# Optimization experiments

Measured on AMD Instinct MI355X. Metric: run time of the kernel, lower is better.

The kernel has to match this reference:

```python
import jax, jax.numpy as jnp
import numpy as np

EPS = 1e-8

def elu_feature_map(x):
    return jax.nn.elu(x) + 1.0

def setup_inputs() -> dict:
    key = jax.random.key(0)
    ks = jax.random.split(key, 5)
    B, S, D = 2, 4096, 1024
    scale = 1.0 / np.sqrt(D).astype(np.float32)
    x = jax.random.normal(ks[0], (B, S, D), dtype=jnp.float32)
    Wq = jax.random.normal(ks[1], (D, D), dtype=jnp.float32) * scale
    Wk = jax.random.normal(ks[2], (D, D), dtype=jnp.float32) * scale
    Wv = jax.random.normal(ks[3], (D, D), dtype=jnp.float32) * scale
    Wo = jax.random.normal(ks[4], (D, D), dtype=jnp.float32) * scale
    return {"x": x, "Wq": Wq, "Wk": Wk, "Wv": Wv, "Wo": Wo}

def reference(x, Wq, Wk, Wv, Wo):
    B, S, D = x.shape
    H = 16
    Dh = D // H
    # projections (nn.Linear with no bias: x @ W.T)
    def proj(W):
        return (x @ W.T).reshape(B, S, H, Dh)
    q = elu_feature_map(proj(Wq))  # [B,S,H,Dh]
    k = elu_feature_map(proj(Wk))
    v = proj(Wv)
    # scan over sequence: carry running kv_sum [B,H,Dh,Dh] and k_sum [B,H,Dh]
    q_t = jnp.moveaxis(q, 1, 0)  # [S,B,H,Dh]
    k_t = jnp.moveaxis(k, 1, 0)
    v_t = jnp.moveaxis(v, 1, 0)

    def step(carry, qkv):
        kv_sum, k_sum = carry
        q_i, k_i, v_i = qkv  # each [B,H,Dh]
        kv_sum = kv_sum + jnp.einsum('bhd,bhe->bhde', k_i, v_i)
        k_sum = k_sum + k_i
        num = jnp.einsum('bhd,bhde->bhe', q_i, kv_sum)
        den = jnp.sum(q_i * k_sum, axis=-1, keepdims=True)
        out_i = num / (den + EPS)
        return (kv_sum, k_sum), out_i

    kv0 = jnp.zeros((B, H, Dh, Dh), dtype=x.dtype)
    ks0 = jnp.zeros((B, H, Dh), dtype=x.dtype)
    _, out = jax.lax.scan(step, (kv0, ks0), (q_t, k_t, v_t))  # out: [S,B,H,Dh]
    out = jnp.moveaxis(out, 0, 1).reshape(B, S, D)
    return out @ Wo.T
```

## Files before the change

kernel.cpp:

```cpp
#include <hip/hip_runtime.h>
#include <math.h>


#define EPSF 1e-8f

typedef unsigned short u16;
typedef unsigned int   u32;
typedef __attribute__((ext_vector_type(8))) short short8v;
typedef __attribute__((ext_vector_type(4))) float f32x4;

__device__ __forceinline__ float elu1(float x){ return x > 0.f ? x + 1.f : __expf(x); }
__device__ __forceinline__ u16 f2bf(float f){
    union{float f; u32 i;} c; c.f = f;
    u32 i = c.i + 0x7FFFu + ((c.i >> 16) & 1u);
    return (u16)(i >> 16);
}
__device__ __forceinline__ float bf2f(u16 v){ union{u32 i; float f;} c; c.i = (u32)v << 16; return c.f; }
__device__ __forceinline__ float bflo(u32 v){ union{u32 i; float f;} c; c.i = v << 16; return c.f; }
__device__ __forceinline__ float bfhi(u32 v){ union{u32 i; float f;} c; c.i = v & 0xffff0000u; return c.f; }
__device__ __forceinline__ void f4a(float4 v, float* a){ a[0]=v.x; a[1]=v.y; a[2]=v.z; a[3]=v.w; }

__device__ __forceinline__ void gload16(const void* g, void* l){
    __builtin_amdgcn_global_load_lds((const __attribute__((address_space(1))) u32*)g,
                                     (__attribute__((address_space(3))) u32*)l, 16, 0, 0);
}

__global__ __launch_bounds__(256) void k_cast5(
    const float* __restrict__ x,  const float* __restrict__ wq,
    const float* __restrict__ wk, const float* __restrict__ wv,
    const float* __restrict__ wo,
    u16* __restrict__ xb, u16* __restrict__ wcat, u16* __restrict__ wob)
{
    size_t i8 = ((size_t)blockIdx.x * 256 + threadIdx.x) * 8;
    const float* s; u16* d; size_t off;
    if      (i8 <  8388608) { s = x;  d = xb;            off = i8; }
    else if (i8 <  9437184) { s = wq; d = wcat;          off = i8 - 8388608; }
    else if (i8 < 10485760) { s = wk; d = wcat + 1048576; off = i8 - 9437184; }
    else if (i8 < 11534336) { s = wv; d = wcat + 2097152; off = i8 - 10485760; }
    else                    { s = wo; d = wob;           off = i8 - 11534336; }
    float4 a = *(const float4*)&s[off];
    float4 b = *(const float4*)&s[off + 4];
    uint4 p;
    p.x = (u32)f2bf(a.x) | ((u32)f2bf(a.y) << 16);
    p.y = (u32)f2bf(a.z) | ((u32)f2bf(a.w) << 16);
    p.z = (u32)f2bf(b.x) | ((u32)f2bf(b.y) << 16);
    p.w = (u32)f2bf(b.z) | ((u32)f2bf(b.w) << 16);
    *(uint4*)&d[off] = p;
}

template<int MODE, int NBY>
__global__ __launch_bounds__(256, 3) void k_gemm9(
    const u16* __restrict__ Ag, const u16* __restrict__ Wg, void* __restrict__ Cv)
{
    __shared__ __align__(16) char dsm[49152];
    const int bid = blockIdx.x;
    const int nid = (bid & 7) * ((64 * NBY) >> 3) + (bid >> 3);
    const int bx  = nid / NBY;
    const int by  = nid % NBY;
    const int m0  = bx * 128;
    const int n0  = by * 128;

    const int tid = threadIdx.x;
    const int l   = tid & 63;
    const int wid = tid >> 6;
    const int wm  = wid >> 1;
    const int wn  = wid & 1;
    const int li  = l & 15;
    const int kgi = l >> 4;

    const int ra0 = wm*64 + li;
    const int offA0 = ((ra0 >> 1) << 7) + (((((ra0 & 1) << 2) | kgi) ^ ((ra0 >> 1) & 7)) << 4);
    const int rb0 = wn*64 + li;
    const int offB0 = ((rb0 >> 1) << 7) + (((((rb0 & 1) << 2) | kgi) ^ ((rb0 >> 1) & 7)) << 4);

    const int sx   = (l & 7) ^ (l >> 3);
    const int rowb = 2*(wid*8 + (l >> 3)) + (sx >> 2);
    const int skg  = (sx & 3) * 8;
    const u16* srcA = Ag + (size_t)(m0 + rowb) * 1024 + skg;
    const u16* srcB = Wg + (size_t)(n0 + rowb) * 1024 + skg;

    f32x4 acc[4][4];
    #pragma unroll
    for (int m = 0; m < 4; ++m)
        #pragma unroll
        for (int n = 0; n < 4; ++n) acc[m][n] = (f32x4){0.f, 0.f, 0.f, 0.f};

    #define ST9(BUF, T) { \
        char* ab = dsm + (BUF)*16384; \
        char* bb = ab + 8192; \
        _Pragma("unroll") for (int j = 0; j < 2; ++j) \
            gload16(srcA + (size_t)j*65536 + (T)*32, ab + j*4096 + wid*1024); \
        _Pragma("unroll") for (int j = 0; j < 2; ++j) \
            gload16(srcB + (size_t)j*65536 + (T)*32, bb + j*4096 + wid*1024); }

    #define CP9(BUF) { \
        const char* Ab = dsm + (BUF)*16384; \
        const char* Bb = Ab + 8192; \
        short8v bfr[4]; \
        _Pragma("unroll") for (int n = 0; n < 4; ++n) bfr[n] = *(const short8v*)(Bb + offB0 + n*1024); \
        __builtin_amdgcn_s_setprio(1); \
        _Pragma("unroll") for (int m = 0; m < 4; ++m) { \
            short8v afr = *(const short8v*)(Ab + offA0 + m*1024); \
            _Pragma("unroll") for (int n = 0; n < 4; ++n) \
                acc[m][n] = __builtin_amdgcn_mfma_f32_16x16x32_bf16(afr, bfr[n], acc[m][n], 0, 0, 0); \
        } \
        __builtin_amdgcn_s_setprio(0); }

    #define STEP9(CUR, STB, TS) { \
        ST9(STB, TS); \
        CP9(CUR); \
        asm volatile("s_waitcnt vmcnt(4)"); \
        __builtin_amdgcn_s_barrier(); }

    ST9(0, 0); ST9(1, 1);
    asm volatile("s_waitcnt vmcnt(4)");
    __builtin_amdgcn_s_barrier();

    #pragma unroll 1
    for (int g = 0; g < 10; ++g) {
        const int t = g * 3;
        STEP9(0, 2, t + 2);
        STEP9(1, 0, t + 3);
        STEP9(2, 1, t + 4);
    }
    CP9(0);
    asm volatile("s_waitcnt vmcnt(0)");
    __builtin_amdgcn_s_barrier();
    CP9(1);
    #undef STEP9
    #undef CP9
    #undef ST9

    const int r0 = m0 + wm*64 + kgi*4;
    if (MODE == 1) {
        const int matrix = by >> 3;
        const bool do_elu = matrix < 2;
        u16* outp = (u16*)Cv + (size_t)matrix * 8388608;
        const int c0 = (by & 7)*128 + wn*64 + li;
        #pragma unroll
        for (int m = 0; m < 4; ++m)
            #pragma unroll
            for (int n = 0; n < 4; ++n)
                #pragma unroll
                for (int r = 0; r < 4; ++r) {
                    float v = acc[m][n][r];
                    if (do_elu) v = elu1(v);
                    outp[(size_t)(r0 + m*16 + r) * 1024 + c0 + n*16] = f2bf(v);
                }
    } else {
        float* outp = (float*)Cv;
        const int c0 = by*128 + wn*64 + li;
        #pragma unroll
        for (int m = 0; m < 4; ++m)
            #pragma unroll
            for (int n = 0; n < 4; ++n)
                #pragma unroll
                for (int r = 0; r < 4; ++r)
                    outp[(size_t)(r0 + m*16 + r) * 1024 + c0 + n*16] = acc[m][n][r];
    }
}

__global__ __launch_bounds__(256) void k_chunksums(
    const u16* __restrict__ Kg, const u16* __restrict__ Vg,
    u16* __restrict__ CKVb, float* __restrict__ CKS)
{
    const int tid = threadIdx.x;
    const int tx = tid & 15, ty = tid >> 4;
    const int c  = blockIdx.x & 63;
    const int bh = blockIdx.x >> 6;
    const int b = bh >> 4, h = bh & 15;
    const int row0 = b * 4096 + c * 64;
    const int col  = h * 64;

    __shared__ float Ks[64][68];
    __shared__ float Vs[64][68];

    #pragma unroll
    for (int r = 0; r < 2; ++r) {
        int idx = tid + r * 256;
        int i = idx >> 3, cg = (idx & 7) << 3;
        uint4 ku = *(const uint4*)&Kg[(size_t)(row0 + i) * 1024 + col + cg];
        uint4 vu = *(const uint4*)&Vg[(size_t)(row0 + i) * 1024 + col + cg];
        Ks[i][cg+0]=bflo(ku.x); Ks[i][cg+1]=bfhi(ku.x);
        Ks[i][cg+2]=bflo(ku.y); Ks[i][cg+3]=bfhi(ku.y);
        Ks[i][cg+4]=bflo(ku.z); Ks[i][cg+5]=bfhi(ku.z);
        Ks[i][cg+6]=bflo(ku.w); Ks[i][cg+7]=bfhi(ku.w);
        Vs[i][cg+0]=bflo(vu.x); Vs[i][cg+1]=bfhi(vu.x);
        Vs[i][cg+2]=bflo(vu.y); Vs[i][cg+3]=bfhi(vu.y);
        Vs[i][cg+4]=bflo(vu.z); Vs[i][cg+5]=bfhi(vu.z);
        Vs[i][cg+6]=bflo(vu.w); Vs[i][cg+7]=bfhi(vu.w);
    }
    __syncthreads();

    float acc[4][4] = {};
    #pragma unroll 8
    for (int i = 0; i < 64; ++i) {
        float kv[4], vv[4];
        f4a(*(const float4*)&Ks[i][ty*4], kv);
        f4a(*(const float4*)&Vs[i][tx*4], vv);
        #pragma unroll
        for (int a = 0; a < 4; ++a)
            #pragma unroll
            for (int e = 0; e < 4; ++e)
                acc[a][e] = fmaf(kv[a], vv[e], acc[a][e]);
    }
    u16* ckv = &CKVb[(size_t)blockIdx.x * 4096];
    #pragma unroll
    for (int e = 0; e < 4; ++e) {
        u32 p0 = (u32)f2bf(acc[0][e]) | ((u32)f2bf(acc[1][e]) << 16);
        u32 p1 = (u32)f2bf(acc[2][e]) | ((u32)f2bf(acc[3][e]) << 16);
        *(uint2*)&ckv[(tx*4 + e) * 64 + ty*4] = make_uint2(p0, p1);
    }

    if (tid < 64) {
        float s = 0.f;
        #pragma unroll 8
        for (int i = 0; i < 64; ++i) s += Ks[i][tid];
        CKS[(size_t)blockIdx.x * 64 + tid] = s;
    }
}

__global__ __launch_bounds__(256) void k_prefix(u16* __restrict__ CKV, float* __restrict__ CKS)
{
    if (blockIdx.x < 512) {
        const int bh = blockIdx.x >> 4;
        const int p  = ((blockIdx.x & 15) << 8) + threadIdx.x;
        const size_t base = (size_t)bh * 64 * 4096 + p;
        float acc = 0.f;
        #pragma unroll
        for (int c = 0; c < 64; ++c) {
            float t = bf2f(CKV[base + (size_t)c * 4096]);
            CKV[base + (size_t)c * 4096] = f2bf(acc);
            acc += t;
        }
    } else {
        const int idx = (blockIdx.x - 512) * 256 + threadIdx.x;
        const int bh = idx >> 6, d = idx & 63;
        const size_t base = (size_t)bh * 64 * 64 + d;
        float v[64];
        #pragma unroll
        for (int c = 0; c < 64; ++c) v[c] = CKS[base + (size_t)c * 64];
        float acc = 0.f;
        #pragma unroll
        for (int c = 0; c < 64; ++c) { float t = v[c]; CKS[base + (size_t)c * 64] = acc; acc += t; }
    }
}

#define LSTR 72
__global__ __launch_bounds__(256) void k_attn2(
    const u16* __restrict__ Qg, const u16* __restrict__ Kg, const u16* __restrict__ Vg,
    const u16* __restrict__ Stg, const float* __restrict__ KSg, u16* __restrict__ AO)
{
    const int tid = threadIdx.x;
    const int l = tid & 63;
    const int w = tid >> 6;
    const int c  = blockIdx.x & 63;
    const int bh = blockIdx.x >> 6;
    const int row0 = (bh >> 4) * 4096 + c * 64;
    const int col  = (bh & 15) * 64;

    __shared__ __align__(16) u16 Qs [64 * LSTR];
    __shared__ __align__(16) u16 Ks [64 * LSTR];
    __shared__ __align__(16) u16 Vt [64 * LSTR];
    __shared__ __align__(16) u16 Sts[64 * LSTR];
    __shared__ __align__(16) u16 Pl [64 * LSTR];
    __shared__ float ksumF[64];
    __shared__ float invdenL[64];

    #pragma unroll
    for (int r = 0; r < 2; ++r) {
        int idx = tid + r * 256;
        int i = idx >> 3, cg = (idx & 7) << 3;
        *(uint4*)&Qs [i*LSTR + cg] = *(const uint4*)&Qg [(size_t)(row0 + i) * 1024 + col + cg];
        *(uint4*)&Ks [i*LSTR + cg] = *(const uint4*)&Kg [(size_t)(row0 + i) * 1024 + col + cg];
        *(uint4*)&Sts[i*LSTR + cg] = *(const uint4*)&Stg[(size_t)blockIdx.x * 4096 + i * 64 + cg];
        uint4 vu = *(const uint4*)&Vg[(size_t)(row0 + i) * 1024 + col + cg];
        Vt[(cg+0)*LSTR + i] = (u16)(vu.x & 0xffff);
        Vt[(cg+1)*LSTR + i] = (u16)(vu.x >> 16);
        Vt[(cg+2)*LSTR + i] = (u16)(vu.y & 0xffff);
        Vt[(cg+3)*LSTR + i] = (u16)(vu.y >> 16);
        Vt[(cg+4)*LSTR + i] = (u16)(vu.z & 0xffff);
        Vt[(cg+5)*LSTR + i] = (u16)(vu.z >> 16);
        Vt[(cg+6)*LSTR + i] = (u16)(vu.w & 0xffff);
        Vt[(cg+7)*LSTR + i] = (u16)(vu.w >> 16);
    }
    if (tid < 64) ksumF[tid] = KSg[(size_t)blockIdx.x * 64 + tid];
    __syncthreads();

    const int li = l & 15;
    const int lg = l >> 4;
    const int i_row = w * 16 + li;

    short8v bq[2];
    #pragma unroll
    for (int kc = 0; kc < 2; ++kc)
        bq[kc] = *(const short8v*)&Qs[i_row * LSTR + lg*8 + kc*32];

    float den = EPSF;
    #pragma unroll
    for (int mj = 0; mj < 4; ++mj) {
        f32x4 sacc = (f32x4){0.f, 0.f, 0.f, 0.f};
        #pragma unroll
        for (int kc = 0; kc < 2; ++kc) {
            short8v ak = *(const short8v*)&Ks[(mj*16 + li) * LSTR + lg*8 + kc*32];
            sacc = __builtin_amdgcn_mfma_f32_16x16x32_bf16(ak, bq[kc], sacc, 0, 0, 0);
        }
        const int jbase = mj*16 + lg*4;
        float pv[4];
        #pragma unroll
        for (int r = 0; r < 4; ++r) {
            float v = sacc[r];
            v = (jbase + r <= i_row) ? v : 0.f;
            den += v;
            pv[r] = v;
        }
        u32 lo = (u32)f2bf(pv[0]) | ((u32)f2bf(pv[1]) << 16);
        u32 hi = (u32)f2bf(pv[2]) | ((u32)f2bf(pv[3]) << 16);
        *(uint2*)&Pl[i_row * LSTR + jbase] = make_uint2(lo, hi);
    }

    {
        const int d0 = lg * 16;
        uint4 q1 = *(const uint4*)&Qs[i_row * LSTR + d0];
        uint4 q2 = *(const uint4*)&Qs[i_row * LSTR + d0 + 8];
        den += bflo(q1.x)*ksumF[d0+0] + bfhi(q1.x)*ksumF[d0+1]
             + bflo(q1.y)*ksumF[d0+2] + bfhi(q1.y)*ksumF[d0+3]
             + bflo(q1.z)*ksumF[d0+4] + bfhi(q1.z)*ksumF[d0+5]
             + bflo(q1.w)*ksumF[d0+6] + bfhi(q1.w)*ksumF[d0+7]
             + bflo(q2.x)*ksumF[d0+8] + bfhi(q2.x)*ksumF[d0+9]
             + bflo(q2.y)*ksumF[d0+10]+ bfhi(q2.y)*ksumF[d0+11]
             + bflo(q2.z)*ksumF[d0+12]+ bfhi(q2.z)*ksumF[d0+13]
             + bflo(q2.w)*ksumF[d0+14]+ bfhi(q2.w)*ksumF[d0+15];
    }
    den += __shfl_xor(den, 16);
    den += __shfl_xor(den, 32);
    if (l < 16) invdenL[w*16 + l] = 1.f / den;

    f32x4 oacc[4];
    #pragma unroll
    for (int ne = 0; ne < 4; ++ne) oacc[ne] = (f32x4){0.f, 0.f, 0.f, 0.f};
    #pragma unroll
    for (int kc = 0; kc < 2; ++kc) {
        short8v ap = *(const short8v*)&Pl[i_row * LSTR + lg*8 + kc*32];
        short8v aq = bq[kc];
        #pragma unroll
        for (int ne = 0; ne < 4; ++ne) {
            short8v bv = *(const short8v*)&Vt [(ne*16 + li) * LSTR + lg*8 + kc*32];
            short8v bs = *(const short8v*)&Sts[(ne*16 + li) * LSTR + lg*8 + kc*32];
            oacc[ne] = __builtin_amdgcn_mfma_f32_16x16x32_bf16(ap, bv, oacc[ne], 0, 0, 0);
            oacc[ne] = __builtin_amdgcn_mfma_f32_16x16x32_bf16(aq, bs, oacc[ne], 0, 0, 0);
        }
    }

    float inv[4];
    #pragma unroll
    for (int r = 0; r < 4; ++r) inv[r] = invdenL[w*16 + lg*4 + r];
    #pragma unroll
    for (int ne = 0; ne < 4; ++ne)
        #pragma unroll
        for (int r = 0; r < 4; ++r)
            Pl[(w*16 + lg*4 + r) * LSTR + ne*16 + li] = f2bf(oacc[ne][r] * inv[r]);

    #pragma unroll
    for (int p = 0; p < 2; ++p) {
        int idx2 = l + p * 64;
        int ro = w*16 + (idx2 >> 3), cg = (idx2 & 7) << 3;
        *(uint4*)&AO[(size_t)(row0 + ro) * 1024 + col + cg] = *(const uint4*)&Pl[ro*LSTR + cg];
    }
}

extern "C" void kernel_launch(void* const* d_in, const int* in_sizes, int n_in,
                              void* d_out, int out_size, void* d_ws, size_t ws_size,
                              hipStream_t stream)
{
    const float* x  = (const float*)d_in[0];
    const float* Wq = (const float*)d_in[1];
    const float* Wk = (const float*)d_in[2];
    const float* Wv = (const float*)d_in[3];
    const float* Wo = (const float*)d_in[4];
    float* out = (float*)d_out;

    char* w = (char*)d_ws;
    u16*   QKVb = (u16*)(w);
    u16*   Qb   = QKVb;
    u16*   Kb   = QKVb + 8388608;
    u16*   Vb   = QKVb + 16777216;
    u16*   xb   = (u16*)(w + 50331648);
    u16*   AOb  = xb;
    u16*   Wcat = (u16*)(w + 67108864);
    u16*   Wob  = (u16*)(w + 73400320);
    u16*   CKVb = (u16*)(w + 75497472);
    float* CKS  = (float*)(w + 92274688);

    k_cast5       <<<6144, 256, 0, stream>>>(x, Wq, Wk, Wv, Wo, xb, Wcat, Wob);
    k_gemm9<1,24> <<<1536, 256, 0, stream>>>(xb, Wcat, (void*)QKVb);
    k_chunksums   <<<2048, 256, 0, stream>>>(Kb, Vb, CKVb, CKS);
    k_prefix      <<<520,  256, 0, stream>>>(CKVb, CKS);
    k_attn2       <<<2048, 256, 0, stream>>>(Qb, Kb, Vb, CKVb, CKS, AOb);
    k_gemm9<3,8>  <<<512,  256, 0, stream>>>(AOb, Wob, (void*)out);
}
```

Before: 147.3 us.

## Use 256-row QKV GEMM tiles and segment-level chunked linear attention

Adds a 256x128-tile QKV projection GEMM with a three-stage LDS pipeline, two blocks per CU, replacing the 128x128 one. The linear attention now uses 256-row segments instead of 64-row chunks. Segment sums are computed with MFMA, the prefix scan shrinks to 16 steps, and the attention kernel updates the running KV state in registers across four sub-chunks. This reduces prefix traffic and state reloads, at the cost of fewer blocks (512) in the attention kernels and a serial dependency inside each block. The segment-sum kernel also contains a leftover dead loop.

```diff
diff --git a/kernel.cpp b/kernel.cpp
--- a/kernel.cpp
+++ b/kernel.cpp
@@ -49,6 +49,118 @@
 }
 
 template<int MODE, int NBY>
+__global__ __launch_bounds__(256, 2) void k_gemm7(
+    const u16* __restrict__ Ag, const u16* __restrict__ Wg, void* __restrict__ Cv)
+{
+    __shared__ __align__(16) char dsm[73728];
+    const int bid = blockIdx.x;
+    const int nid = (bid & 7) * ((32 * NBY) >> 3) + (bid >> 3);
+    const int bx  = nid / NBY;
+    const int by  = nid % NBY;
+    const int m0  = bx * 256;
+    const int n0  = by * 128;
+
+    const int tid = threadIdx.x;
+    const int l   = tid & 63;
+    const int wid = tid >> 6;
+    const int wm  = wid >> 1;
+    const int wn  = wid & 1;
+    const int li  = l & 15;
+    const int kgi = l >> 4;
+
+    const int ra0 = wm*128 + li;
+    const int offA0 = (ra0 >> 1)*128 + (((((ra0 & 1) << 2) | kgi) ^ ((ra0 >> 1) & 7)) << 4);
+    const int rb0 = wn*64 + li;
+    const int offB0 = (rb0 >> 1)*128 + (((((rb0 & 1) << 2) | kgi) ^ ((rb0 >> 1) & 7)) << 4);
+
+    const int sx   = (l & 7) ^ (l >> 3);
+    const int rowb = 2*(wid*8 + (l >> 3)) + (sx >> 2);
+    const int skg  = (sx & 3) * 8;
+    const u16* srcA = Ag + (size_t)(m0 + rowb) * 1024 + skg;
+    const u16* srcB = Wg + (size_t)(n0 + rowb) * 1024 + skg;
+
+    f32x4 acc[8][4];
+    #pragma unroll
+    for (int m = 0; m < 8; ++m)
+        #pragma unroll
+        for (int n = 0; n < 4; ++n) acc[m][n] = (f32x4){0.f, 0.f, 0.f, 0.f};
+
+    #define ST7(BUF, T) { \
+        char* ab = dsm + (BUF)*24576; \
+        char* bb = ab + 16384; \
+        _Pragma("unroll") for (int j = 0; j < 4; ++j) \
+            gload16(srcA + (size_t)j*65536 + (T)*32, ab + j*4096 + wid*1024); \
+        _Pragma("unroll") for (int j = 0; j < 2; ++j) \
+            gload16(srcB + (size_t)j*65536 + (T)*32, bb + j*4096 + wid*1024); }
+
+    #define CP7(BUF) { \
+        const char* Ab = dsm + (BUF)*24576; \
+        const char* Bb = Ab + 16384; \
+        short8v bfr[4]; \
+        _Pragma("unroll") for (int n = 0; n < 4; ++n) bfr[n] = *(const short8v*)(Bb + offB0 + n*1024); \
+        __builtin_amdgcn_s_setprio(1); \
+        _Pragma("unroll") for (int m = 0; m < 8; ++m) { \
+            short8v afr = *(const short8v*)(Ab + offA0 + m*1024); \
+            _Pragma("unroll") for (int n = 0; n < 4; ++n) \
+                acc[m][n] = __builtin_amdgcn_mfma_f32_16x16x32_bf16(afr, bfr[n], acc[m][n], 0, 0, 0); \
+        } \
+        __builtin_amdgcn_s_setprio(0); }
+
+    #define STEP7(CUR, STB, TS) { \
+        ST7(STB, TS); \
+        CP7(CUR); \
+        asm volatile("s_waitcnt vmcnt(6)"); \
+        __builtin_amdgcn_s_barrier(); }
+
+    ST7(0, 0); ST7(1, 1);
+    asm volatile("s_waitcnt vmcnt(6)");
+    __builtin_amdgcn_s_barrier();
+
+    #pragma unroll 1
+    for (int g = 0; g < 10; ++g) {
+        const int t = g * 3;
+        STEP7(0, 2, t + 2);
+        STEP7(1, 0, t + 3);
+        STEP7(2, 1, t + 4);
+    }
+    CP7(0);
+    asm volatile("s_waitcnt vmcnt(0)");
+    __builtin_amdgcn_s_barrier();
+    CP7(1);
+    #undef STEP7
+    #undef CP7
+    #undef ST7
+
+    const int r0 = m0 + wm*128 + kgi*4;
+    if (MODE == 1) {
+        const int matrix = by >> 3;
+        const bool do_elu = matrix < 2;
+        u16* outp = (u16*)Cv + (size_t)matrix * 8388608;
+        const int c0 = (by & 7)*128 + wn*64 + li;
+        #pragma unroll
+        for (int m = 0; m < 8; ++m)
+            #pragma unroll
+            for (int n = 0; n < 4; ++n)
+                #pragma unroll
+                for (int r = 0; r < 4; ++r) {
+                    float v = acc[m][n][r];
+                    if (do_elu) v = elu1(v);
+                    outp[(size_t)(r0 + m*16 + r) * 1024 + c0 + n*16] = f2bf(v);
+                }
+    } else {
+        float* outp = (float*)Cv;
+        const int c0 = by*128 + wn*64 + li;
+        #pragma unroll
+        for (int m = 0; m < 8; ++m)
+            #pragma unroll
+            for (int n = 0; n < 4; ++n)
+                #pragma unroll
+                for (int r = 0; r < 4; ++r)
+                    outp[(size_t)(r0 + m*16 + r) * 1024 + c0 + n*16] = acc[m][n][r];
+    }
+}
+
+template<int MODE, int NBY>
 __global__ __launch_bounds__(256, 3) void k_gemm9(
     const u16* __restrict__ Ag, const u16* __restrict__ Wg, void* __restrict__ Cv)
 {
@@ -160,212 +272,293 @@
     }
 }
 
-__global__ __launch_bounds__(256) void k_chunksums(
+#define LSTR 72
+__global__ __launch_bounds__(256) void k_segsums(
     const u16* __restrict__ Kg, const u16* __restrict__ Vg,
-    u16* __restrict__ CKVb, float* __restrict__ CKS)
+    u16* __restrict__ SegKV, float* __restrict__ SegKS)
 {
     const int tid = threadIdx.x;
-    const int tx = tid & 15, ty = tid >> 4;
-    const int c  = blockIdx.x & 63;
-    const int bh = blockIdx.x >> 6;
-    const int b = bh >> 4, h = bh & 15;
-    const int row0 = b * 4096 + c * 64;
-    const int col  = h * 64;
-
-    __shared__ float Ks[64][68];
-    __shared__ float Vs[64][68];
+    const int l = tid & 63;
+    const int w = tid >> 6;
+    const int bh  = blockIdx.x >> 4;
+    const int seg = blockIdx.x & 15;
+    const int row0 = (bh >> 4) * 4096 + seg * 256;
+    const int col  = (bh & 15) * 64;
+    const int li = l & 15;
+    const int lg = l >> 4;
+
+    __shared__ __align__(16) u16 Kt[64 * LSTR];
+    __shared__ __align__(16) u16 Vt[64 * LSTR];
+    __shared__ float ksPart[4][64];
+
+    f32x4 Stacc[4];
+    #pragma unroll
+    for (int nd = 0; nd < 4; ++nd) Stacc[nd] = (f32x4){0.f, 0.f, 0.f, 0.f};
+    float ksAcc = 0.f;
+
+    for (int cc = 0; cc < 4; ++cc) {
+        const int rc = row0 + cc * 64;
+        #pragma unroll
+        for (int r = 0; r < 2; ++r) {
+            int idx = tid + r * 256;
+            int i = idx >> 3, cg = (idx & 7) << 3;
+            uint4 ku = *(const uint4*)&Kg[(size_t)(rc + i) * 1024 + col + cg];
+            uint4 vu = *(const uint4*)&Vg[(size_t)(rc + i) * 1024 + col + cg];
+            Kt[(cg+0)*LSTR + i] = (u16)(ku.x & 0xffff);
+            Kt[(cg+1)*LSTR + i] = (u16)(ku.x >> 16);
+            Kt[(cg+2)*LSTR + i] = (u16)(ku.y & 0xffff);
+            Kt[(cg+3)*LSTR + i] = (u16)(ku.y >> 16);
+            Kt[(cg+4)*LSTR + i] = (u16)(ku.z & 0xffff);
+            Kt[(cg+5)*LSTR + i] = (u16)(ku.z >> 16);
+            Kt[(cg+6)*LSTR + i] = (u16)(ku.w & 0xffff);
+            Kt[(cg+7)*LSTR + i] = (u16)(ku.w >> 16);
+            Vt[(cg+0)*LSTR + i] = (u16)(vu.x & 0xffff);
+            Vt[(cg+1)*LSTR + i] = (u16)(vu.x >> 16);
+            Vt[(cg+2)*LSTR + i] = (u16)(vu.y & 0xffff);
+            Vt[(cg+3)*LSTR + i] = (u16)(vu.y >> 16);
+            Vt[(cg+4)*LSTR + i] = (u16)(vu.z & 0xffff);
+            Vt[(cg+5)*LSTR + i] = (u16)(vu.z >> 16);
+            Vt[(cg+6)*LSTR + i] = (u16)(vu.w & 0xffff);
+            Vt[(cg+7)*LSTR + i] = (u16)(vu.w >> 16);
+        }
+        __syncthreads();
+        #pragma unroll
+        for (int kc = 0; kc < 2; ++kc) {
+            short8v av = *(const short8v*)&Vt[(w*16 + li) * LSTR + lg*8 + kc*32];
+            #pragma unroll
+            for (int nd = 0; nd < 4; ++nd) {
+                short8v bk = *(const short8v*)&Kt[(nd*16 + li) * LSTR + lg*8 + kc*32];
+                Stacc[nd] = __builtin_amdgcn_mfma_f32_16x16x32_bf16(av, bk, Stacc[nd], 0, 0, 0);
+            }
+        }
+        {
+            const int d = tid & 63, q = tid >> 6;
+            float s = 0.f;
+            #pragma unroll
+            for (int ii = 0; ii < 16; ++ii) s += bf2f(Kt[d * LSTR + 0] * 0 + Kt[(d)*LSTR + 0]);
+            s = 0.f;
+            #pragma unroll
+            for (int ii = 0; ii < 16; ++ii) s += bf2f(Kt[d * LSTR + q*16 + ii]);
+            ksPart[q][d] = s;
+        }
+        __syncthreads();
+        if (tid < 64) ksAcc += ksPart[0][tid] + ksPart[1][tid] + ksPart[2][tid] + ksPart[3][tid];
+        __syncthreads();
+    }
+
+    u16* out = &SegKV[(size_t)blockIdx.x * 4096];
+    #pragma unroll
+    for (int nd = 0; nd < 4; ++nd)
+        #pragma unroll
+        for (int r = 0; r < 4; ++r)
+            out[(16*w + lg*4 + r) * 64 + nd*16 + li] = f2bf(Stacc[nd][r]);
+    if (tid < 64) SegKS[(size_t)blockIdx.x * 64 + tid] = ksAcc;
+}
+
+__global__ __launch_bounds__(256) void k_prefix2(u16* __restrict__ SegKV, float* __restrict__ SegKS)
+{
+    if (blockIdx.x < 512) {
+        const int bh = blockIdx.x >> 4;
+        const int p  = ((blockIdx.x & 15) << 8) + threadIdx.x;
+        const size_t base = (size_t)bh * 16 * 4096 + p;
+        float acc = 0.f;
+        #pragma unroll
+        for (int s = 0; s < 16; ++s) {
+            float t = bf2f(SegKV[base + (size_t)s * 4096]);
+            SegKV[base + (size_t)s * 4096] = f2bf(acc);
+            acc += t;
+        }
+    } else {
+        const int idx = (blockIdx.x - 512) * 256 + threadIdx.x;
+        const int bh = idx >> 6, d = idx & 63;
+        const size_t base = (size_t)bh * 16 * 64 + d;
+        float acc = 0.f;
+        #pragma unroll
+        for (int s = 0; s < 16; ++s) {
+            float t = SegKS[base + (size_t)s * 64];
+            SegKS[base + (size_t)s * 64] = acc;
+            acc += t;
+        }
+    }
+}
+
+__global__ __launch_bounds__(256) void k_attn3(
+    const u16* __restrict__ Qg, const u16* __restrict__ Kg, const u16* __restrict__ Vg,
+    const u16* __restrict__ SegKVp, const float* __restrict__ SegKSp, u16* __restrict__ AO)
+{
+    const int tid = threadIdx.x;
+    const int l = tid & 63;
+    const int w = tid >> 6;
+    const int bh  = blockIdx.x >> 4;
+    const int seg = blockIdx.x & 15;
+    const int row0 = (bh >> 4) * 4096 + seg * 256;
+    const int col  = (bh & 15) * 64;
+    const int li = l & 15;
+    const int lg = l >> 4;
+    const int i_row = w * 16 + li;
+
+    __shared__ __align__(16) u16 Qs [64 * LSTR];
+    __shared__ __align__(16) u16 Ks [64 * LSTR];
+    __shared__ __align__(16) u16 Kt [64 * LSTR];
+    __shared__ __align__(16) u16 Vt [64 * LSTR];
+    __shared__ __align__(16) u16 Sts[64 * LSTR];
+    __shared__ __align__(16) u16 Pl [64 * LSTR];
+    __shared__ float ksum[64];
+    __shared__ float ksPart[4][64];
+    __shared__ float invdenL[64];
 
     #pragma unroll
     for (int r = 0; r < 2; ++r) {
         int idx = tid + r * 256;
         int i = idx >> 3, cg = (idx & 7) << 3;
-        uint4 ku = *(const uint4*)&Kg[(size_t)(row0 + i) * 1024 + col + cg];
-        uint4 vu = *(const uint4*)&Vg[(size_t)(row0 + i) * 1024 + col + cg];
-        Ks[i][cg+0]=bflo(ku.x); Ks[i][cg+1]=bfhi(ku.x);
-        Ks[i][cg+2]=bflo(ku.y); Ks[i][cg+3]=bfhi(ku.y);
-        Ks[i][cg+4]=bflo(ku.z); Ks[i][cg+5]=bfhi(ku.z);
-        Ks[i][cg+6]=bflo(ku.w); Ks[i][cg+7]=bfhi(ku.w);
-        Vs[i][cg+0]=bflo(vu.x); Vs[i][cg+1]=bfhi(vu.x);
-        Vs[i][cg+2]=bflo(vu.y); Vs[i][cg+3]=bfhi(vu.y);
-        Vs[i][cg+4]=bflo(vu.z); Vs[i][cg+5]=bfhi(vu.z);
-        Vs[i][cg+6]=bflo(vu.w); Vs[i][cg+7]=bfhi(vu.w);
-    }
+        *(uint4*)&Sts[i*LSTR + cg] = *(const uint4*)&SegKVp[(size_t)blockIdx.x * 4096 + i * 64 + cg];
+    }
+    if (tid < 64) ksum[tid] = SegKSp[(size_t)blockIdx.x * 64 + tid];
     __syncthreads();
 
-    float acc[4][4] = {};
-    #pragma unroll 8
-    for (int i = 0; i < 64; ++i) {
-        float kv[4], vv[4];
-        f4a(*(const float4*)&Ks[i][ty*4], kv);
-        f4a(*(const float4*)&Vs[i][tx*4], vv);
-        #pragma unroll
-        for (int a = 0; a < 4; ++a)
-            #pragma unroll
-            for (int e = 0; e < 4; ++e)
-                acc[a][e] = fmaf(kv[a], vv[e], acc[a][e]);
-    }
-    u16* ckv = &CKVb[(size_t)blockIdx.x * 4096];
+    f32x4 Stacc[4];
     #pragma unroll
-    for (int e = 0; e < 4; ++e) {
-        u32 p0 = (u32)f2bf(acc[0][e]) | ((u32)f2bf(acc[1][e]) << 16);
-        u32 p1 = (u32)f2bf(acc[2][e]) | ((u32)f2bf(acc[3][e]) << 16);
-        *(uint2*)&ckv[(tx*4 + e) * 64 + ty*4] = make_uint2(p0, p1);
-    }
-
-    if (tid < 64) {
-        float s = 0.f;
-        #pragma unroll 8
-        for (int i = 0; i < 64; ++i) s += Ks[i][tid];
-        CKS[(size_t)blockIdx.x * 64 + tid] = s;
-    }
-}
-
-__global__ __launch_bounds__(256) void k_prefix(u16* __restrict__ CKV, float* __restrict__ CKS)
-{
-    if (blockIdx.x < 512) {
-        const int bh = blockIdx.x >> 4;
-        const int p  = ((blockIdx.x & 15) << 8) + threadIdx.x;
-        const size_t base = (size_t)bh * 64 * 4096 + p;
-        float acc = 0.f;
-        #pragma unroll
-        for (int c = 0; c < 64; ++c) {
-            float t = bf2f(CKV[base + (size_t)c * 4096]);
-            CKV[base + (size_t)c * 4096] = f2bf(acc);
-            acc += t;
-        }
-    } else {
-        const int idx = (blockIdx.x - 512) * 256 + threadIdx.x;
-        const int bh = idx >> 6, d = idx & 63;
-        const size_t base = (size_t)bh * 64 * 64 + d;
-        float v[64];
-        #pragma unroll
-        for (int c = 0; c < 64; ++c) v[c] = CKS[base + (size_t)c * 64];
-        float acc = 0.f;
-        #pragma unroll
-        for (int c = 0; c < 64; ++c) { float t = v[c]; CKS[base + (size_t)c * 64] = acc; acc += t; }
-    }
-}
-
-#define LSTR 72
-__global__ __launch_bounds__(256) void k_attn2(
-    const u16* __restrict__ Qg, const u16* __restrict__ Kg, const u16* __restrict__ Vg,
-    const u16* __restrict__ Stg, const float* __restrict__ KSg, u16* __restrict__ AO)
-{
-    const int tid = threadIdx.x;
-    const int l = tid & 63;
-    const int w = tid >> 6;
-    const int c  = blockIdx.x & 63;
-    const int bh = blockIdx.x >> 6;
-    const int row0 = (bh >> 4) * 4096 + c * 64;
-    const int col  = (bh & 15) * 64;
-
-    __shared__ __align__(16) u16 Qs [64 * LSTR];
-    __shared__ __align__(16) u16 Ks [64 * LSTR];
-    __shared__ __align__(16) u16 Vt [64 * LSTR];
-    __shared__ __align__(16) u16 Sts[64 * LSTR];
-    __shared__ __align__(16) u16 Pl [64 * LSTR];
-    __shared__ float ksumF[64];
-    __shared__ float invdenL[64];
-
-    #pragma unroll
-    for (int r = 0; r < 2; ++r) {
-        int idx = tid + r * 256;
-        int i = idx >> 3, cg = (idx & 7) << 3;
-        *(uint4*)&Qs [i*LSTR + cg] = *(const uint4*)&Qg [(size_t)(row0 + i) * 1024 + col + cg];
-        *(uint4*)&Ks [i*LSTR + cg] = *(const uint4*)&Kg [(size_t)(row0 + i) * 1024 + col + cg];
-        *(uint4*)&Sts[i*LSTR + cg] = *(const uint4*)&Stg[(size_t)blockIdx.x * 4096 + i * 64 + cg];
-        uint4 vu = *(const uint4*)&Vg[(size_t)(row0 + i) * 1024 + col + cg];
-        Vt[(cg+0)*LSTR + i] = (u16)(vu.x & 0xffff);
-        Vt[(cg+1)*LSTR + i] = (u16)(vu.x >> 16);
-        Vt[(cg+2)*LSTR + i] = (u16)(vu.y & 0xffff);
-        Vt[(cg+3)*LSTR + i] = (u16)(vu.y >> 16);
-        Vt[(cg+4)*LSTR + i] = (u16)(vu.z & 0xffff);
-        Vt[(cg+5)*LSTR + i] = (u16)(vu.z >> 16);
-        Vt[(cg+6)*LSTR + i] = (u16)(vu.w & 0xffff);
-        Vt[(cg+7)*LSTR + i] = (u16)(vu.w >> 16);
-    }
-    if (tid < 64) ksumF[tid] = KSg[(size_t)blockIdx.x * 64 + tid];
-    __syncthreads();
-
-    const int li = l & 15;
-    const int lg = l >> 4;
-    const int i_row = w * 16 + li;
-
-    short8v bq[2];
-    #pragma unroll
-    for (int kc = 0; kc < 2; ++kc)
-        bq[kc] = *(const short8v*)&Qs[i_row * LSTR + lg*8 + kc*32];
-
-    float den = EPSF;
-    #pragma unroll
-    for (int mj = 0; mj < 4; ++mj) {
-        f32x4 sacc = (f32x4){0.f, 0.f, 0.f, 0.f};
+    for (int nd = 0; nd < 4; ++nd)
+        #pragma unroll
+        for (int r = 0; r < 4; ++r)
+            Stacc[nd][r] = bf2f(Sts[(16*w + lg*4 + r) * LSTR + nd*16 + li]);
+
+    for (int cc = 0; cc < 4; ++cc) {
+        const int rc = row0 + cc * 64;
+        #pragma unroll
+        for (int r = 0; r < 2; ++r) {
+            int idx = tid + r * 256;
+            int i = idx >> 3, cg = (idx & 7) << 3;
+            *(uint4*)&Qs[i*LSTR + cg] = *(const uint4*)&Qg[(size_t)(rc + i) * 1024 + col + cg];
+            uint4 ku = *(const uint4*)&Kg[(size_t)(rc + i) * 1024 + col + cg];
+            uint4 vu = *(const uint4*)&Vg[(size_t)(rc + i) * 1024 + col + cg];
+            *(uint4*)&Ks[i*LSTR + cg] = ku;
+            Kt[(cg+0)*LSTR + i] = (u16)(ku.x & 0xffff);
+            Kt[(cg+1)*LSTR + i] = (u16)(ku.x >> 16);
+            Kt[(cg+2)*LSTR + i] = (u16)(ku.y & 0xffff);
+            Kt[(cg+3)*LSTR + i] = (u16)(ku.y >> 16);
+            Kt[(cg+4)*LSTR + i] = (u16)(ku.z & 0xffff);
+            Kt[(cg+5)*LSTR + i] = (u16)(ku.z >> 16);
+            Kt[(cg+6)*LSTR + i] = (u16)(ku.w & 0xffff);
+            Kt[(cg+7)*LSTR + i] = (u16)(ku.w >> 16);
+            Vt[(cg+0)*LSTR + i] = (u16)(vu.x & 0xffff);
+            Vt[(cg+1)*LSTR + i] = (u16)(vu.x >> 16);
+            Vt[(cg+2)*LSTR + i] = (u16)(vu.y & 0xffff);
+            Vt[(cg+3)*LSTR + i] = (u16)(vu.y >> 16);
+            Vt[(cg+4)*LSTR + i] = (u16)(vu.z & 0xffff);
+            Vt[(cg+5)*LSTR + i] = (u16)(vu.z >> 16);
+            Vt[(cg+6)*LSTR + i] = (u16)(vu.w & 0xffff);
+            Vt[(cg+7)*LSTR + i] = (u16)(vu.w >> 16);
+        }
+        __syncthreads();
+
+        short8v bq[2];
+        #pragma unroll
+        for (int kc = 0; kc < 2; ++kc)
+            bq[kc] = *(const short8v*)&Qs[i_row * LSTR + lg*8 + kc*32];
+
+        float den = EPSF;
+        #pragma unroll
+        for (int mj = 0; mj < 4; ++mj) {
+            f32x4 sacc = (f32x4){0.f, 0.f, 0.f, 0.f};
+            #pragma unroll
+            for (int kc = 0; kc < 2; ++kc) {
+                short8v ak = *(const short8v*)&Ks[(mj*16 + li) * LSTR + lg*8 + kc*32];
+                sacc = __builtin_amdgcn_mfma_f32_16x16x32_bf16(ak, bq[kc], sacc, 0, 0, 0);
+            }
+            const int jbase = mj*16 + lg*4;
+            float pv[4];
+            #pragma unroll
+            for (int r = 0; r < 4; ++r) {
+                float v = sacc[r];
+                v = (jbase + r <= i_row) ? v : 0.f;
+                den += v;
+                pv[r] = v;
+            }
+            u32 lo = (u32)f2bf(pv[0]) | ((u32)f2bf(pv[1]) << 16);
+            u32 hi = (u32)f2bf(pv[2]) | ((u32)f2bf(pv[3]) << 16);
+            *(uint2*)&Pl[i_row * LSTR + jbase] = make_uint2(lo, hi);
+        }
+        {
+            const int d0 = lg * 16;
+            uint4 q1 = *(const uint4*)&Qs[i_row * LSTR + d0];
+            uint4 q2 = *(const uint4*)&Qs[i_row * LSTR + d0 + 8];
+            den += bflo(q1.x)*ksum[d0+0] + bfhi(q1.x)*ksum[d0+1]
+                 + bflo(q1.y)*ksum[d0+2] + bfhi(q1.y)*ksum[d0+3]
+                 + bflo(q1.z)*ksum[d0+4] + bfhi(q1.z)*ksum[d0+5]
+                 + bflo(q1.w)*ksum[d0+6] + bfhi(q1.w)*ksum[d0+7]
+                 + bflo(q2.x)*ksum[d0+8] + bfhi(q2.x)*ksum[d0+9]
+                 + bflo(q2.y)*ksum[d0+10]+ bfhi(q2.y)*ksum[d0+11]
+                 + bflo(q2.z)*ksum[d0+12]+ bfhi(q2.z)*ksum[d0+13]
+                 + bflo(q2.w)*ksum[d0+14]+ bfhi(q2.w)*ksum[d0+15];
+        }
+        den += __shfl_xor(den, 16);
+        den += __shfl_xor(den, 32);
+        if (l < 16) invdenL[w*16 + l] = 1.f / den;
+
+        if (cc < 3) {
+            const int d = tid & 63, q = tid >> 6;
+            float s = 0.f;
+            #pragma unroll
+            for (int ii = 0; ii < 16; ++ii) s += bf2f(Kt[d * LSTR + q*16 + ii]);
+            ksPart[q][d] = s;
+        }
+        __syncthreads();
+
+        f32x4 oacc[4];
+        #pragma unroll
+        for (int ne = 0; ne < 4; ++ne) oacc[ne] = (f32x4){0.f, 0.f, 0.f, 0.f};
         #pragma unroll
         for (int kc = 0; kc < 2; ++kc) {
-            short8v ak = *(const short8v*)&Ks[(mj*16 + li) * LSTR + lg*8 + kc*32];
-            sacc = __builtin_amdgcn_mfma_f32_16x16x32_bf16(ak, bq[kc], sacc, 0, 0, 0);
-        }
-        const int jbase = mj*16 + lg*4;
-        float pv[4];
-        #pragma unroll
-        for (int r = 0; r < 4; ++r) {
-            float v = sacc[r];
-            v = (jbase + r <= i_row) ? v : 0.f;
-            den += v;
-            pv[r] = v;
-        }
-        u32 lo = (u32)f2bf(pv[0]) | ((u32)f2bf(pv[1]) << 16);
-        u32 hi = (u32)f2bf(pv[2]) | ((u32)f2bf(pv[3]) << 16);
-        *(uint2*)&Pl[i_row * LSTR + jbase] = make_uint2(lo, hi);
-    }
-
-    {
-        const int d0 = lg * 16;
-        uint4 q1 = *(const uint4*)&Qs[i_row * LSTR + d0];
-        uint4 q2 = *(const uint4*)&Qs[i_row * LSTR + d0 + 8];
-        den += bflo(q1.x)*ksumF[d0+0] + bfhi(q1.x)*ksumF[d0+1]
-             + bflo(q1.y)*ksumF[d0+2] + bfhi(q1.y)*ksumF[d0+3]
-             + bflo(q1.z)*ksumF[d0+4] + bfhi(q1.z)*ksumF[d0+5]
-             + bflo(q1.w)*ksumF[d0+6] + bfhi(q1.w)*ksumF[d0+7]
-             + bflo(q2.x)*ksumF[d0+8] + bfhi(q2.x)*ksumF[d0+9]
-             + bflo(q2.y)*ksumF[d0+10]+ bfhi(q2.y)*ksumF[d0+11]
-             + bflo(q2.z)*ksumF[d0+12]+ bfhi(q2.z)*ksumF[d0+13]
-             + bflo(q2.w)*ksumF[d0+14]+ bfhi(q2.w)*ksumF[d0+15];
-    }
-    den += __shfl_xor(den, 16);
-    den += __shfl_xor(den, 32);
-    if (l < 16) invdenL[w*16 + l] = 1.f / den;
-
-    f32x4 oacc[4];
-    #pragma unroll
-    for (int ne = 0; ne < 4; ++ne) oacc[ne] = (f32x4){0.f, 0.f, 0.f, 0.f};
-    #pragma unroll
-    for (int kc = 0; kc < 2; ++kc) {
-        short8v ap = *(const short8v*)&Pl[i_row * LSTR + lg*8 + kc*32];
-        short8v aq = bq[kc];
-        #pragma unroll
-        for (int ne = 0; ne < 4; ++ne) {
-            short8v bv = *(const short8v*)&Vt [(ne*16 + li) * LSTR + lg*8 + kc*32];
-            short8v bs = *(const short8v*)&Sts[(ne*16 + li) * LSTR + lg*8 + kc*32];
-            oacc[ne] = __builtin_amdgcn_mfma_f32_16x16x32_bf16(ap, bv, oacc[ne], 0, 0, 0);
-            oacc[ne] = __builtin_amdgcn_mfma_f32_16x16x32_bf16(aq, bs, oacc[ne], 0, 0, 0);
-        }
-    }
-
-    float inv[4];
-    #pragma unroll
-    for (int r = 0; r < 4; ++r) inv[r] = invdenL[w*16 + lg*4 + r];
-    #pragma unroll
-    for (int ne = 0; ne < 4; ++ne)
-        #pragma unroll
-        for (int r = 0; r < 4; ++r)
-            Pl[(w*16 + lg*4 + r) * LSTR + ne*16 + li] = f2bf(oacc[ne][r] * inv[r]);
-
-    #pragma unroll
-    for (int p = 0; p < 2; ++p) {
-        int idx2 = l + p * 64;
-        int ro = w*16 + (idx2 >> 3), cg = (idx2 & 7) << 3;
-        *(uint4*)&AO[(size_t)(row0 + ro) * 1024 + col + cg] = *(const uint4*)&Pl[ro*LSTR + cg];
+            short8v ap = *(const short8v*)&Pl[i_row * LSTR + lg*8 + kc*32];
+            short8v aq = bq[kc];
+            #pragma unroll
+            for (int ne = 0; ne < 4; ++ne) {
+                short8v bv = *(const short8v*)&Vt [(ne*16 + li) * LSTR + lg*8 + kc*32];
+                short8v bs = *(const short8v*)&Sts[(ne*16 + li) * LSTR + lg*8 + kc*32];
+                oacc[ne] = __builtin_amdgcn_mfma_f32_16x16x32_bf16(ap, bv, oacc[ne], 0, 0, 0);
+                oacc[ne] = __builtin_amdgcn_mfma_f32_16x16x32_bf16(aq, bs, oacc[ne], 0, 0, 0);
+            }
+        }
+        if (cc < 3 && tid < 64)
+            ksum[tid] += ksPart[0][tid] + ksPart[1][tid] + ksPart[2][tid] + ksPart[3][tid];
+
+        if (cc < 3) {
+            #pragma unroll
+            for (int kc = 0; kc < 2; ++kc) {
+                short8v av = *(const short8v*)&Vt[(w*16 + li) * LSTR + lg*8 + kc*32];
+                #pragma unroll
+                for (int nd = 0; nd < 4; ++nd) {
+                    short8v bk = *(const short8v*)&Kt[(nd*16 + li) * LSTR + lg*8 + kc*32];
+                    Stacc[nd] = __builtin_amdgcn_mfma_f32_16x16x32_bf16(av, bk, Stacc[nd], 0, 0, 0);
+                }
+            }
+        }
+
+        float inv[4];
+        #pragma unroll
+        for (int r = 0; r < 4; ++r) inv[r] = invdenL[w*16 + lg*4 + r];
+        #pragma unroll
+        for (int ne = 0; ne < 4; ++ne)
+            #pragma unroll
+            for (int r = 0; r < 4; ++r)
+                Pl[(w*16 + lg*4 + r) * LSTR + ne*16 + li] = f2bf(oacc[ne][r] * inv[r]);
+        #pragma unroll
+        for (int p = 0; p < 2; ++p) {
+            int idx2 = l + p * 64;
+            int ro = w*16 + (idx2 >> 3), cg = (idx2 & 7) << 3;
+            *(uint4*)&AO[(size_t)(rc + ro) * 1024 + col + cg] = *(const uint4*)&Pl[ro*LSTR + cg];
+        }
+
+        __syncthreads();
+        if (cc < 3) {
+            #pragma unroll
+            for (int nd = 0; nd < 4; ++nd)
+                #pragma unroll
+                for (int r = 0; r < 4; ++r)
+                    Sts[(16*w + lg*4 + r) * LSTR + nd*16 + li] = f2bf(Stacc[nd][r]);
+            __syncthreads();
+        }
     }
 }
 
@@ -381,21 +574,21 @@
     float* out = (float*)d_out;
 
     char* w = (char*)d_ws;
-    u16*   QKVb = (u16*)(w);
-    u16*   Qb   = QKVb;
-    u16*   Kb   = QKVb + 8388608;
-    u16*   Vb   = QKVb + 16777216;
-    u16*   xb   = (u16*)(w + 50331648);
-    u16*   AOb  = xb;
-    u16*   Wcat = (u16*)(w + 67108864);
-    u16*   Wob  = (u16*)(w + 73400320);
-    u16*   CKVb = (u16*)(w + 75497472);
-    float* CKS  = (float*)(w + 92274688);
+    u16*   QKVb  = (u16*)(w);
+    u16*   Qb    = QKVb;
+    u16*   Kb    = QKVb + 8388608;
+    u16*   Vb    = QKVb + 16777216;
+    u16*   xb    = (u16*)(w + 50331648);
+    u16*   AOb   = xb;
+    u16*   Wcat  = (u16*)(w + 67108864);
+    u16*   Wob   = (u16*)(w + 73400320);
+    u16*   SegKV = (u16*)(w + 75497472);
+    float* SegKS = (float*)(w + 79691776);
 
     k_cast5       <<<6144, 256, 0, stream>>>(x, Wq, Wk, Wv, Wo, xb, Wcat, Wob);
-    k_gemm9<1,24> <<<1536, 256, 0, stream>>>(xb, Wcat, (void*)QKVb);
-    k_chunksums   <<<2048, 256, 0, stream>>>(Kb, Vb, CKVb, CKS);
-    k_prefix      <<<520,  256, 0, stream>>>(CKVb, CKS);
-    k_attn2       <<<2048, 256, 0, stream>>>(Qb, Kb, Vb, CKVb, CKS, AOb);
+    k_gemm7<1,24> <<<768,  256, 0, stream>>>(xb, Wcat, (void*)QKVb);
+    k_segsums     <<<512,  256, 0, stream>>>(Kb, Vb, SegKV, SegKS);
+    k_prefix2     <<<520,  256, 0, stream>>>(SegKV, SegKS);
+    k_attn3       <<<512,  256, 0, stream>>>(Qb, Kb, Vb, SegKV, SegKS, AOb);
     k_gemm9<3,8>  <<<512,  256, 0, stream>>>(AOb, Wob, (void*)out);
 }
```

New measurement: 132.3 us. 10.2% less time.
